# Kernel optimization log

Hardware: AMD Instinct MI355X
Metric: run time of the kernel (lower is better)

## Reference

```python
import jax, jax.numpy as jnp
import numpy as np

N_HEAD = 16
WINDOW = 256
GLOBAL = 32


def _sparse_mask(T):
    # local window of +/- WINDOW//2 plus global rows/cols for first GLOBAL tokens
    i = jnp.arange(T)
    local = jnp.abs(i[:, None] - i[None, :]) <= (WINDOW // 2)
    glob = (i[:, None] < GLOBAL) | (i[None, :] < GLOBAL)
    return local | glob  # [T, T] bool


def setup_inputs() -> dict:
    key = jax.random.key(0)
    k1, k2, k3 = jax.random.split(key, 3)
    B, T, C = 1, 4096, 1024
    scale = 0.02
    return {
        "x": jax.random.normal(k1, (B, T, C), dtype=jnp.float32),
        "W_attn": jax.random.normal(k2, (C, 3 * C), dtype=jnp.float32) * scale,
        "b_attn": jnp.zeros((3 * C,), dtype=jnp.float32),
        "W_proj": jax.random.normal(k3, (C, C), dtype=jnp.float32) * scale,
        "b_proj": jnp.zeros((C,), dtype=jnp.float32),
    }


def reference(x, W_attn, b_attn, W_proj, b_proj):
    B, T, C = x.shape
    H = N_HEAD
    D = C // H

    qkv = x @ W_attn + b_attn  # [B, T, 3C]
    q, k, v = jnp.split(qkv, 3, axis=-1)
    # [B, H, T, D]
    q = q.reshape(B, T, H, D).transpose(0, 2, 1, 3)
    k = k.reshape(B, T, H, D).transpose(0, 2, 1, 3)
    v = v.reshape(B, T, H, D).transpose(0, 2, 1, 3)

    mask = _sparse_mask(T)  # [T, T]
    att = jnp.einsum("bhqd,bhkd->bhqk", q, k) * (1.0 / np.sqrt(D))
    neg = jnp.finfo(att.dtype).min
    att = jnp.where(mask, att, neg)
    att = jax.nn.softmax(att, axis=-1)
    y = jnp.einsum("bhqk,bhkd->bhqd", att, v)  # [B, H, T, D]
    y = y.transpose(0, 2, 1, 3).reshape(B, T, C)
    return y @ W_proj + b_proj
```

## Files before the change

### kernel.cpp

```cpp
#include <hip/hip_runtime.h>
#include <hip/hip_bf16.h>
#include <math.h>

#define T_SEQ 4096
#define C_DIM 1024
#define H_HEADS 16
#define D_HEAD 64
#define QKVW 3072
#define WIN_HALF 128
#define GLOBAL_TOK 32

typedef __attribute__((ext_vector_type(8))) short bf16x8;
typedef __attribute__((ext_vector_type(4))) float f32x4;

__device__ __forceinline__ float bf2f(unsigned short u) {
    union { unsigned int i; float f; } c; c.i = ((unsigned int)u) << 16; return c.f;
}
__device__ __forceinline__ unsigned short f2bf(float f) {
    union { float f; unsigned int i; } c; c.f = f;
    return (unsigned short)((c.i + 0x7fffu + ((c.i >> 16) & 1u)) >> 16);
}

__device__ __forceinline__ void gll16(const unsigned short* g, unsigned short* l) {
    __builtin_amdgcn_global_load_lds(
        (const __attribute__((address_space(1))) void*)g,
        (__attribute__((address_space(3))) void*)l, 16, 0, 0);
}

__global__ __launch_bounds__(256) void cvt_f32_bf16_kernel(
    const float* __restrict__ src, unsigned short* __restrict__ dst, int n4)
{
    int idx = blockIdx.x * 256 + threadIdx.x;
    if (idx < n4) {
        float4 v = ((const float4*)src)[idx];
        ushort4 o;
        o.x = f2bf(v.x); o.y = f2bf(v.y); o.z = f2bf(v.z); o.w = f2bf(v.w);
        ((ushort4*)dst)[idx] = o;
    }
}

__global__ __launch_bounds__(256) void cvt_transpose_kernel(
    const float* __restrict__ src, unsigned short* __restrict__ dst,
    int R, int Ncols)
{
    __shared__ unsigned short tile[32][36];
    const int r0 = blockIdx.y * 32, c0 = blockIdx.x * 32;
    const int t = threadIdx.x;
    const int rr = t >> 3, cq = (t & 7) * 4;
    float4 v = *(const float4*)(src + (size_t)(r0 + rr) * Ncols + c0 + cq);
    tile[rr][cq + 0] = f2bf(v.x); tile[rr][cq + 1] = f2bf(v.y);
    tile[rr][cq + 2] = f2bf(v.z); tile[rr][cq + 3] = f2bf(v.w);
    __syncthreads();
    const int cc = t >> 3, rq = (t & 7) * 4;
    ushort4 o;
    o.x = tile[rq + 0][cc]; o.y = tile[rq + 1][cc];
    o.z = tile[rq + 2][cc]; o.w = tile[rq + 3][cc];
    *(ushort4*)(dst + (size_t)(c0 + cc) * R + r0 + rq) = o;
}

__global__ __launch_bounds__(256) void transpose_v_kernel(
    const unsigned short* __restrict__ qkv, unsigned short* __restrict__ vT)
{
    __shared__ unsigned short tile[32][36];
    const int c0 = blockIdx.x * 32;
    const int t0 = blockIdx.y * 32;
    const int t = threadIdx.x;
    const int rr = t >> 3, cq = (t & 7) * 4;
    ushort4 v = *(const ushort4*)(qkv + (size_t)(t0 + rr) * QKVW + 2 * C_DIM + c0 + cq);
    tile[rr][cq + 0] = v.x; tile[rr][cq + 1] = v.y;
    tile[rr][cq + 2] = v.z; tile[rr][cq + 3] = v.w;
    __syncthreads();
    const int cc = t >> 3, rq = (t & 7) * 4;
    ushort4 o;
    o.x = tile[rq + 0][cc]; o.y = tile[rq + 1][cc];
    o.z = tile[rq + 2][cc]; o.w = tile[rq + 3][cc];
    *(ushort4*)(vT + (size_t)(c0 + cc) * T_SEQ + t0 + rq) = o;
}

template<int OUT_BF16>
__global__ __launch_bounds__(256) void gemm_nt_kernel(
    const unsigned short* __restrict__ A,
    const unsigned short* __restrict__ Bt,
    const float* __restrict__ bias,
    void* __restrict__ Cv, int M, int N, int K)
{
    __shared__ unsigned short As[128 * 32];
    __shared__ unsigned short Bs[128 * 32];
    const int tid = threadIdx.x;
    const int w = tid >> 6, lane = tid & 63;
    const int quad = lane >> 4, r16 = lane & 15;
    const int m0 = blockIdx.y * 128, n0 = blockIdx.x * 128;
    const int wm = (w & 1) * 64, wn = (w >> 1) * 64;

    f32x4 acc[4][4];
    #pragma unroll
    for (int i = 0; i < 4; ++i)
        #pragma unroll
        for (int j = 0; j < 4; ++j) acc[i][j] = (f32x4){0.f, 0.f, 0.f, 0.f};

    const unsigned short* Ab = A + (size_t)m0 * K;
    const unsigned short* Bb = Bt + (size_t)n0 * K;

    for (int k0 = 0; k0 < K; k0 += 32) {
        __syncthreads();
        #pragma unroll
        for (int i = 0; i < 2; ++i) {
            const int chunk = w * 128 + i * 64 + lane;
            const int row = chunk >> 2, kc = (chunk & 3) * 8;
            gll16(Ab + (size_t)row * K + k0 + kc, &As[(w * 2 + i) * 512]);
            gll16(Bb + (size_t)row * K + k0 + kc, &Bs[(w * 2 + i) * 512]);
        }
        asm volatile("s_waitcnt vmcnt(0)" ::: "memory");
        __builtin_amdgcn_sched_barrier(0);
        __syncthreads();

        bf16x8 af[4], bf_[4];
        #pragma unroll
        for (int t = 0; t < 4; ++t) {
            af[t]  = *(const bf16x8*)&As[(wm + t * 16 + r16) * 32 + quad * 8];
            bf_[t] = *(const bf16x8*)&Bs[(wn + t * 16 + r16) * 32 + quad * 8];
        }
        #pragma unroll
        for (int mt = 0; mt < 4; ++mt)
            #pragma unroll
            for (int nt = 0; nt < 4; ++nt)
                acc[mt][nt] = __builtin_amdgcn_mfma_f32_16x16x32_bf16(
                    af[mt], bf_[nt], acc[mt][nt], 0, 0, 0);
    }

    #pragma unroll
    for (int nt = 0; nt < 4; ++nt) {
        const int col = n0 + wn + nt * 16 + r16;
        const float bv = bias[col];
        #pragma unroll
        for (int mt = 0; mt < 4; ++mt)
            #pragma unroll
            for (int reg = 0; reg < 4; ++reg) {
                const int row = m0 + wm + mt * 16 + quad * 4 + reg;
                if (OUT_BF16)
                    ((unsigned short*)Cv)[(size_t)row * N + col] = f2bf(acc[mt][nt][reg] + bv);
                else
                    ((float*)Cv)[(size_t)row * N + col] = acc[mt][nt][reg] + bv;
            }
    }
}

#define PT_STRIDE 72
#define NSLOT 8
#define PROW 72

struct KVbuf { bf16x8 kl[4], kh[4], vl[4], vh[4]; };

#define LOAD_KV(C0, B)                                                         \
  {                                                                            \
    const unsigned short* kr_ = kb + (size_t)((C0) + n) * QKVW + quad * 8;     \
    _Pragma("unroll")                                                          \
    for (int g = 0; g < 4; ++g) {                                              \
      B.kl[g] = *(const bf16x8*)(kr_ + (size_t)(g * 16) * QKVW);               \
      B.kh[g] = *(const bf16x8*)(kr_ + (size_t)(g * 16) * QKVW + 32);          \
    }                                                                          \
    const unsigned short* vr_ = vb + (size_t)n * T_SEQ + (C0) + quad * 8;      \
    _Pragma("unroll")                                                          \
    for (int d = 0; d < 4; ++d) {                                              \
      B.vl[d] = *(const bf16x8*)(vr_ + (size_t)(d * 16) * T_SEQ);              \
      B.vh[d] = *(const bf16x8*)(vr_ + (size_t)(d * 16) * T_SEQ + 32);         \
    }                                                                          \
  }

#define PROC_TILE(ITV, CUR, NXT)                                               \
  {                                                                            \
    const int it_ = (ITV);                                                     \
    const int c0 = dense ? (split * 512 + it_ * 64)                            \
                         : (it_ == 0 ? 0 : wlo + (it_ - 1) * 64);              \
    f32x4 St[4];                                                               \
    _Pragma("unroll")                                                          \
    for (int g = 0; g < 4; ++g) {                                              \
      St[g] = __builtin_amdgcn_mfma_f32_16x16x32_bf16(CUR.kl[g], q0, Zf, 0, 0, 0); \
      St[g] = __builtin_amdgcn_mfma_f32_16x16x32_bf16(CUR.kh[g], q1, St[g], 0, 0, 0); \
    }                                                                          \
    if (it_ + 1 < n_tiles) {                                                   \
      const int c0n_ = dense ? (split * 512 + (it_ + 1) * 64)                  \
                             : (it_ == 0 ? wlo : c0 + 64);                     \
      LOAD_KV(c0n_, NXT);                                                      \
    }                                                                          \
    float mm = -INFINITY;                                                      \
    const bool interior_ =                                                     \
        dense || (it_ != 0 && c0 >= rowbase - 113 && c0 <= rowbase + 65);      \
    if (interior_) {                                                           \
      _Pragma("unroll")                                                        \
      for (int g = 0; g < 4; ++g)                                              \
        _Pragma("unroll")                                                      \
        for (int r = 0; r < 4; ++r) {                                          \
          const float v = St[g][r] * 0.125f;                                   \
          St[g][r] = v; mm = fmaxf(mm, v);                                     \
        }                                                                      \
    } else if (it_ == 0 && rowbase >= 192) {                                   \
      _Pragma("unroll")                                                        \
      for (int g = 0; g < 2; ++g)                                              \
        _Pragma("unroll")                                                      \
        for (int r = 0; r < 4; ++r) {                                          \
          const float v = St[g][r] * 0.125f;                                   \
          St[g][r] = v; mm = fmaxf(mm, v);                                     \
        }                                                                      \
      _Pragma("unroll")                                                        \
      for (int g = 2; g < 4; ++g)                                              \
        _Pragma("unroll")                                                      \
        for (int r = 0; r < 4; ++r) St[g][r] = -INFINITY;                      \
    } else {                                                                   \
      _Pragma("unroll")                                                        \
      for (int g = 0; g < 4; ++g)                                              \
        _Pragma("unroll")                                                      \
        for (int r = 0; r < 4; ++r) {                                          \
          float v = St[g][r] * 0.125f;                                         \
          const int col = c0 + g * 16 + quad * 4 + r;                          \
          int dd = row - col; dd = dd < 0 ? -dd : dd;                          \
          if (!(col < GLOBAL_TOK || dd <= WIN_HALF)) v = -INFINITY;            \
          St[g][r] = v; mm = fmaxf(mm, v);                                     \
        }                                                                      \
    }                                                                          \
    mm = fmaxf(mm, __shfl_xor(mm, 16));                                        \
    mm = fmaxf(mm, __shfl_xor(mm, 32));                                        \
    const float mn = fmaxf(m_run, mm);                                         \
    const float mnf = (mn == -INFINITY) ? 0.f : mn;                            \
    const float al = __expf(m_run - mnf);                                      \
    float rs = 0.f;                                                            \
    _Pragma("unroll")                                                          \
    for (int g = 0; g < 4; ++g) {                                              \
      const float e0 = __expf(St[g][0] - mnf);                                 \
      const float e1 = __expf(St[g][1] - mnf);                                 \
      const float e2 = __expf(St[g][2] - mnf);                                 \
      const float e3 = __expf(St[g][3] - mnf);                                 \
      rs += (e0 + e1) + (e2 + e3);                                             \
      const unsigned int p01 = f2bf(e0) | ((unsigned int)f2bf(e1) << 16);      \
      const unsigned int p23 = f2bf(e2) | ((unsigned int)f2bf(e3) << 16);      \
      *(unsigned int*)&myPt[n * PT_STRIDE + g * 16 + quad * 4] = p01;          \
      *(unsigned int*)&myPt[n * PT_STRIDE + g * 16 + quad * 4 + 2] = p23;      \
    }                                                                          \
    rs += __shfl_xor(rs, 16);                                                  \
    rs += __shfl_xor(rs, 32);                                                  \
    l_run = l_run * al + rs;                                                   \
    m_run = mn;                                                                \
    _Pragma("unroll")                                                          \
    for (int d = 0; d < 4; ++d)                                                \
      _Pragma("unroll")                                                        \
      for (int r = 0; r < 4; ++r) O[d][r] *= al;                               \
    asm volatile("s_waitcnt lgkmcnt(0)" ::: "memory");                         \
    __builtin_amdgcn_sched_barrier(0);                                         \
    _Pragma("unroll")                                                          \
    for (int kg = 0; kg < 2; ++kg) {                                           \
      bf16x8 pf_ = *(const bf16x8*)&myPt[n * PT_STRIDE + kg * 32 + quad * 8];  \
      _Pragma("unroll")                                                        \
      for (int d = 0; d < 4; ++d)                                              \
        O[d] = __builtin_amdgcn_mfma_f32_16x16x32_bf16(                        \
            kg ? CUR.vh[d] : CUR.vl[d], pf_, O[d], 0, 0, 0);                   \
    }                                                                          \
  }

__global__ __launch_bounds__(256, 2) void sparse_attn_mfma(
    const unsigned short* __restrict__ qkv,
    const unsigned short* __restrict__ vT,
    unsigned short* __restrict__ y,
    float* __restrict__ part)
{
    __shared__ unsigned short Pt[4][16 * PT_STRIDE];
    const int tid = threadIdx.x;
    const int w = tid >> 6, lane = tid & 63;
    const int quad = lane >> 4, n = lane & 15;
    const int bid = blockIdx.x;

    int h, rowbase, split = -1, rt = 0;
    if (bid < 1024) {
        h = bid & 15;
        const int rtile = (bid >> 4) * 4 + w;
        if (rtile < 2) return;
        rowbase = rtile * 16;
    } else {
        const int idx = bid - 1024;
        h = idx & 15;
        const int u = (idx >> 4) * 4 + w;
        rt = u >> 3; split = u & 7;
        rowbase = rt * 16;
    }
    const bool dense = split >= 0;

    int wlo = 0, n_tiles;
    if (dense) n_tiles = 8;
    else {
        int t0 = (rowbase - WIN_HALF) & ~63; if (t0 < 64) t0 = 64;
        wlo = t0;
        int whi = rowbase + 16 + WIN_HALF; if (whi > T_SEQ) whi = T_SEQ;
        n_tiles = 1 + (whi - wlo + 63) / 64;
    }

    const unsigned short* qp = qkv + (size_t)(rowbase + n) * QKVW + h * 64 + quad * 8;
    bf16x8 q0 = *(const bf16x8*)qp;
    bf16x8 q1 = *(const bf16x8*)(qp + 32);

    const unsigned short* kb = qkv + C_DIM + h * 64;
    const unsigned short* vb = vT + (size_t)h * 64 * T_SEQ;
    unsigned short* myPt = Pt[w];

    f32x4 O[4];
    #pragma unroll
    for (int i = 0; i < 4; ++i) O[i] = (f32x4){0.f, 0.f, 0.f, 0.f};
    float m_run = -INFINITY, l_run = 0.f;
    const int row = rowbase + n;
    const f32x4 Zf = (f32x4){0.f, 0.f, 0.f, 0.f};

    KVbuf b0, b1;
    {
        const int c00 = dense ? (split * 512) : 0;
        LOAD_KV(c00, b0);
    }
    int it = 0;
    for (;;) {
        PROC_TILE(it, b0, b1);
        if (++it >= n_tiles) break;
        PROC_TILE(it, b1, b0);
        if (++it >= n_tiles) break;
    }

    if (!dense) {
        const float invL = 1.f / l_run;
        #pragma unroll
        for (int dblk = 0; dblk < 4; ++dblk)
            #pragma unroll
            for (int r = 0; r < 4; ++r)
                y[(size_t)row * C_DIM + h * 64 + dblk * 16 + quad * 4 + r] =
                    f2bf(O[dblk][r] * invL);
    } else {
        float* pb = part + ((size_t)(h * 2 + rt) * NSLOT + split) * 16 * PROW;
        #pragma unroll
        for (int dblk = 0; dblk < 4; ++dblk)
            #pragma unroll
            for (int r = 0; r < 4; ++r)
                pb[n * PROW + dblk * 16 + quad * 4 + r] = O[dblk][r];
        if (quad == 0) {
            pb[n * PROW + 64] = m_run;
            pb[n * PROW + 65] = l_run;
        }
    }
}

__global__ __launch_bounds__(64) void attn_combine(
    const float* __restrict__ part, unsigned short* __restrict__ y)
{
    const int d = threadIdx.x;
    const int h = blockIdx.x >> 1, rt = blockIdx.x & 1;
    const float* base = part + (size_t)(h * 2 + rt) * NSLOT * 16 * PROW;
    for (int row = 0; row < 16; ++row) {
        float M = -INFINITY;
        for (int sl = 0; sl < NSLOT; ++sl)
            M = fmaxf(M, base[(size_t)sl * 16 * PROW + row * PROW + 64]);
        float L = 0.f, Od = 0.f;
        for (int sl = 0; sl < NSLOT; ++sl) {
            const float* p = base + (size_t)sl * 16 * PROW + row * PROW;
            const float s = __expf(p[64] - M);
            L += p[65] * s;
            Od += p[d] * s;
        }
        y[(size_t)(rt * 16 + row) * C_DIM + h * 64 + d] = f2bf(Od / L);
    }
}

extern "C" void kernel_launch(void* const* d_in, const int* in_sizes, int n_in,
                              void* d_out, int out_size, void* d_ws, size_t ws_size,
                              hipStream_t stream) {
    const float* x  = (const float*)d_in[0];
    const float* Wa = (const float*)d_in[1];
    const float* ba = (const float*)d_in[2];
    const float* Wp = (const float*)d_in[3];
    const float* bp = (const float*)d_in[4];
    float* out = (float*)d_out;

    unsigned short* xb   = (unsigned short*)d_ws;
    unsigned short* Wabt = xb   + (size_t)T_SEQ * C_DIM;
    unsigned short* Wpbt = Wabt + (size_t)C_DIM * QKVW;
    unsigned short* qkv  = Wpbt + (size_t)C_DIM * C_DIM;
    unsigned short* yat  = qkv  + (size_t)T_SEQ * QKVW;
    unsigned short* vT = xb;
    float* part = (float*)Wabt;

    const int n_x = T_SEQ * C_DIM;
    cvt_f32_bf16_kernel<<<n_x / 4 / 256, 256, 0, stream>>>(x, xb, n_x / 4);
    cvt_transpose_kernel<<<dim3(QKVW / 32, C_DIM / 32), 256, 0, stream>>>(
        Wa, Wabt, C_DIM, QKVW);
    cvt_transpose_kernel<<<dim3(C_DIM / 32, C_DIM / 32), 256, 0, stream>>>(
        Wp, Wpbt, C_DIM, C_DIM);

    gemm_nt_kernel<1><<<dim3(QKVW / 128, T_SEQ / 128), 256, 0, stream>>>(
        xb, Wabt, ba, qkv, T_SEQ, QKVW, C_DIM);

    transpose_v_kernel<<<dim3(C_DIM / 32, T_SEQ / 32), 256, 0, stream>>>(qkv, vT);

    const int nBlocks = 1024 + 64;
    sparse_attn_mfma<<<nBlocks, 256, 0, stream>>>(qkv, vT, yat, part);
    attn_combine<<<H_HEADS * 2, 64, 0, stream>>>(part, yat);

    gemm_nt_kernel<0><<<dim3(C_DIM / 128, T_SEQ / 128), 256, 0, stream>>>(
        yat, Wpbt, bp, out, T_SEQ, C_DIM, C_DIM);
}
```

Measured before the change: 224.0 us.

## Share K/V tiles across warps via swizzled double-buffered LDS in windowed attention

Before this change, each warp in the windowed (non-dense) path loaded its own K/V fragments straight from global memory. Now the four warps of a block, which cover 64 consecutive rows, share a union window of K/V tiles. The block stages those tiles cooperatively into XOR-swizzled, double-buffered LDS, with register prefetch of the next tile and __syncthreads between tiles. This cuts redundant global traffic, and the launch-bounds occupancy hint rises from 2 to 3 blocks per SM. In exchange, each warp now iterates over the larger union window, which adds some wasted MFMA work, and every tile pays a block-wide barrier. The dense global-row path is split out unchanged.

```diff
diff --git a/kernel.cpp b/kernel.cpp
--- a/kernel.cpp
+++ b/kernel.cpp
@@ -25,6 +25,10 @@
     __builtin_amdgcn_global_load_lds(
         (const __attribute__((address_space(1))) void*)g,
         (__attribute__((address_space(3))) void*)l, 16, 0, 0);
+}
+
+__device__ __forceinline__ int swz(int row, int chunk) {
+    return row * 64 + ((chunk ^ (row & 7)) * 8);
 }
 
 __global__ __launch_bounds__(256) void cvt_f32_bf16_kernel(
@@ -150,6 +154,7 @@
 #define PROW 72
 
 struct KVbuf { bf16x8 kl[4], kh[4], vl[4], vh[4]; };
+struct StReg { bf16x8 a, b, c, d; };
 
 #define LOAD_KV(C0, B)                                                         \
   {                                                                            \
@@ -167,57 +172,7 @@
     }                                                                          \
   }
 
-#define PROC_TILE(ITV, CUR, NXT)                                               \
-  {                                                                            \
-    const int it_ = (ITV);                                                     \
-    const int c0 = dense ? (split * 512 + it_ * 64)                            \
-                         : (it_ == 0 ? 0 : wlo + (it_ - 1) * 64);              \
-    f32x4 St[4];                                                               \
-    _Pragma("unroll")                                                          \
-    for (int g = 0; g < 4; ++g) {                                              \
-      St[g] = __builtin_amdgcn_mfma_f32_16x16x32_bf16(CUR.kl[g], q0, Zf, 0, 0, 0); \
-      St[g] = __builtin_amdgcn_mfma_f32_16x16x32_bf16(CUR.kh[g], q1, St[g], 0, 0, 0); \
-    }                                                                          \
-    if (it_ + 1 < n_tiles) {                                                   \
-      const int c0n_ = dense ? (split * 512 + (it_ + 1) * 64)                  \
-                             : (it_ == 0 ? wlo : c0 + 64);                     \
-      LOAD_KV(c0n_, NXT);                                                      \
-    }                                                                          \
-    float mm = -INFINITY;                                                      \
-    const bool interior_ =                                                     \
-        dense || (it_ != 0 && c0 >= rowbase - 113 && c0 <= rowbase + 65);      \
-    if (interior_) {                                                           \
-      _Pragma("unroll")                                                        \
-      for (int g = 0; g < 4; ++g)                                              \
-        _Pragma("unroll")                                                      \
-        for (int r = 0; r < 4; ++r) {                                          \
-          const float v = St[g][r] * 0.125f;                                   \
-          St[g][r] = v; mm = fmaxf(mm, v);                                     \
-        }                                                                      \
-    } else if (it_ == 0 && rowbase >= 192) {                                   \
-      _Pragma("unroll")                                                        \
-      for (int g = 0; g < 2; ++g)                                              \
-        _Pragma("unroll")                                                      \
-        for (int r = 0; r < 4; ++r) {                                          \
-          const float v = St[g][r] * 0.125f;                                   \
-          St[g][r] = v; mm = fmaxf(mm, v);                                     \
-        }                                                                      \
-      _Pragma("unroll")                                                        \
-      for (int g = 2; g < 4; ++g)                                              \
-        _Pragma("unroll")                                                      \
-        for (int r = 0; r < 4; ++r) St[g][r] = -INFINITY;                      \
-    } else {                                                                   \
-      _Pragma("unroll")                                                        \
-      for (int g = 0; g < 4; ++g)                                              \
-        _Pragma("unroll")                                                      \
-        for (int r = 0; r < 4; ++r) {                                          \
-          float v = St[g][r] * 0.125f;                                         \
-          const int col = c0 + g * 16 + quad * 4 + r;                          \
-          int dd = row - col; dd = dd < 0 ? -dd : dd;                          \
-          if (!(col < GLOBAL_TOK || dd <= WIN_HALF)) v = -INFINITY;            \
-          St[g][r] = v; mm = fmaxf(mm, v);                                     \
-        }                                                                      \
-    }                                                                          \
+#define SOFTMAX_P_UPDATE(StV)                                                  \
     mm = fmaxf(mm, __shfl_xor(mm, 16));                                        \
     mm = fmaxf(mm, __shfl_xor(mm, 32));                                        \
     const float mn = fmaxf(m_run, mm);                                         \
@@ -226,10 +181,10 @@
     float rs = 0.f;                                                            \
     _Pragma("unroll")                                                          \
     for (int g = 0; g < 4; ++g) {                                              \
-      const float e0 = __expf(St[g][0] - mnf);                                 \
-      const float e1 = __expf(St[g][1] - mnf);                                 \
-      const float e2 = __expf(St[g][2] - mnf);                                 \
-      const float e3 = __expf(St[g][3] - mnf);                                 \
+      const float e0 = __expf(StV[g][0] - mnf);                                \
+      const float e1 = __expf(StV[g][1] - mnf);                                \
+      const float e2 = __expf(StV[g][2] - mnf);                                \
+      const float e3 = __expf(StV[g][3] - mnf);                                \
       rs += (e0 + e1) + (e2 + e3);                                             \
       const unsigned int p01 = f2bf(e0) | ((unsigned int)f2bf(e1) << 16);      \
       const unsigned int p23 = f2bf(e2) | ((unsigned int)f2bf(e3) << 16);      \
@@ -243,7 +198,30 @@
     _Pragma("unroll")                                                          \
     for (int d = 0; d < 4; ++d)                                                \
       _Pragma("unroll")                                                        \
-      for (int r = 0; r < 4; ++r) O[d][r] *= al;                               \
+      for (int r = 0; r < 4; ++r) O[d][r] *= al;
+
+#define PROC_TILE(ITV, CUR, NXT)                                               \
+  {                                                                            \
+    const int it_ = (ITV);                                                     \
+    const int c0 = split * 512 + it_ * 64;                                     \
+    f32x4 St[4];                                                               \
+    _Pragma("unroll")                                                          \
+    for (int g = 0; g < 4; ++g) {                                              \
+      St[g] = __builtin_amdgcn_mfma_f32_16x16x32_bf16(CUR.kl[g], q0, Zf, 0, 0, 0); \
+      St[g] = __builtin_amdgcn_mfma_f32_16x16x32_bf16(CUR.kh[g], q1, St[g], 0, 0, 0); \
+    }                                                                          \
+    if (it_ + 1 < n_tiles) {                                                   \
+      LOAD_KV(c0 + 64, NXT);                                                   \
+    }                                                                          \
+    float mm = -INFINITY;                                                      \
+    _Pragma("unroll")                                                          \
+    for (int g = 0; g < 4; ++g)                                                \
+      _Pragma("unroll")                                                        \
+      for (int r = 0; r < 4; ++r) {                                            \
+        const float v = St[g][r] * 0.125f;                                     \
+        St[g][r] = v; mm = fmaxf(mm, v);                                       \
+      }                                                                        \
+    SOFTMAX_P_UPDATE(St)                                                       \
     asm volatile("s_waitcnt lgkmcnt(0)" ::: "memory");                         \
     __builtin_amdgcn_sched_barrier(0);                                         \
     _Pragma("unroll")                                                          \
@@ -256,79 +234,195 @@
     }                                                                          \
   }
 
-__global__ __launch_bounds__(256, 2) void sparse_attn_mfma(
+#define STAGE_LOAD(C0, R)                                                      \
+  { const int c0s_ = (C0);                                                     \
+    R.a = *(const bf16x8*)(kb + (size_t)(c0s_ + srow) * QKVW + scol * 8);      \
+    R.b = *(const bf16x8*)(kb + (size_t)(c0s_ + srow + 32) * QKVW + scol * 8); \
+    R.c = *(const bf16x8*)(vb + (size_t)srow * T_SEQ + c0s_ + scol * 8);       \
+    R.d = *(const bf16x8*)(vb + (size_t)(srow + 32) * T_SEQ + c0s_ + scol * 8); }
+
+#define STAGE_WRITE(BUF, R)                                                    \
+  { *(bf16x8*)&Ks[BUF][kdst0] = R.a;                                           \
+    *(bf16x8*)&Ks[BUF][kdst1] = R.b;                                           \
+    *(bf16x8*)&Vs[BUF][kdst0] = R.c;                                           \
+    *(bf16x8*)&Vs[BUF][kdst1] = R.d; }
+
+#define WTILE(ITV, BUF, RW, RL)                                                \
+  {                                                                            \
+    const int it_ = (ITV);                                                     \
+    const int c0 = (it_ == 0) ? 0 : (blo + (it_ - 1) * 64);                    \
+    if (activeW) {                                                             \
+      bf16x8 kl[4], kh[4];                                                     \
+      _Pragma("unroll")                                                        \
+      for (int g = 0; g < 4; ++g) {                                            \
+        kl[g] = *(const bf16x8*)&Ks[BUF][swz(n + g * 16, quad)];               \
+        kh[g] = *(const bf16x8*)&Ks[BUF][swz(n + g * 16, quad + 4)];           \
+      }                                                                        \
+      f32x4 St[4];                                                             \
+      _Pragma("unroll")                                                        \
+      for (int g = 0; g < 4; ++g) {                                            \
+        St[g] = __builtin_amdgcn_mfma_f32_16x16x32_bf16(kl[g], q0, Zf, 0, 0, 0); \
+        St[g] = __builtin_amdgcn_mfma_f32_16x16x32_bf16(kh[g], q1, St[g], 0, 0, 0); \
+      }                                                                        \
+      float mm = -INFINITY;                                                    \
+      if (it_ != 0 && c0 >= rowbase - 113 && c0 <= rowbase + 65) {             \
+        _Pragma("unroll")                                                      \
+        for (int g = 0; g < 4; ++g)                                            \
+          _Pragma("unroll")                                                    \
+          for (int r = 0; r < 4; ++r) {                                        \
+            const float v = St[g][r] * 0.125f;                                 \
+            St[g][r] = v; mm = fmaxf(mm, v);                                   \
+          }                                                                    \
+      } else if (it_ == 0 && rowbase >= 192) {                                 \
+        _Pragma("unroll")                                                      \
+        for (int g = 0; g < 2; ++g)                                            \
+          _Pragma("unroll")                                                    \
+          for (int r = 0; r < 4; ++r) {                                        \
+            const float v = St[g][r] * 0.125f;                                 \
+            St[g][r] = v; mm = fmaxf(mm, v);                                   \
+          }                                                                    \
+        _Pragma("unroll")                                                      \
+        for (int g = 2; g < 4; ++g)                                            \
+          _Pragma("unroll")                                                    \
+          for (int r = 0; r < 4; ++r) St[g][r] = -INFINITY;                    \
+      } else {                                                                 \
+        _Pragma("unroll")                                                      \
+        for (int g = 0; g < 4; ++g)                                            \
+          _Pragma("unroll")                                                    \
+          for (int r = 0; r < 4; ++r) {                                        \
+            float v = St[g][r] * 0.125f;                                       \
+            const int col = c0 + g * 16 + quad * 4 + r;                        \
+            int dd = row - col; dd = dd < 0 ? -dd : dd;                        \
+            if (!(col < GLOBAL_TOK || dd <= WIN_HALF)) v = -INFINITY;          \
+            St[g][r] = v; mm = fmaxf(mm, v);                                   \
+          }                                                                    \
+      }                                                                        \
+      SOFTMAX_P_UPDATE(St)                                                     \
+      bf16x8 vl[4], vh[4];                                                     \
+      _Pragma("unroll")                                                        \
+      for (int d = 0; d < 4; ++d) {                                            \
+        vl[d] = *(const bf16x8*)&Vs[BUF][swz(n + d * 16, quad)];               \
+        vh[d] = *(const bf16x8*)&Vs[BUF][swz(n + d * 16, quad + 4)];           \
+      }                                                                        \
+      asm volatile("s_waitcnt lgkmcnt(0)" ::: "memory");                       \
+      __builtin_amdgcn_sched_barrier(0);                                       \
+      _Pragma("unroll")                                                        \
+      for (int kg = 0; kg < 2; ++kg) {                                         \
+        bf16x8 pf_ = *(const bf16x8*)&myPt[n * PT_STRIDE + kg * 32 + quad * 8];\
+        _Pragma("unroll")                                                      \
+        for (int d = 0; d < 4; ++d)                                            \
+          O[d] = __builtin_amdgcn_mfma_f32_16x16x32_bf16(                      \
+              kg ? vh[d] : vl[d], pf_, O[d], 0, 0, 0);                         \
+      }                                                                        \
+    }                                                                          \
+    if (it_ + 1 < NT) {                                                        \
+      asm volatile("s_waitcnt vmcnt(0)" ::: "memory");                         \
+      __builtin_amdgcn_sched_barrier(0);                                       \
+      STAGE_WRITE((BUF) ^ 1, RW);                                              \
+      if (it_ + 2 < NT) { STAGE_LOAD(blo + (it_ + 1) * 64, RL); }              \
+      __syncthreads();                                                         \
+    }                                                                          \
+  }
+
+__global__ __launch_bounds__(256, 3) void sparse_attn_mfma(
     const unsigned short* __restrict__ qkv,
     const unsigned short* __restrict__ vT,
     unsigned short* __restrict__ y,
     float* __restrict__ part)
 {
+    __shared__ unsigned short Ks[2][64 * 64];
+    __shared__ unsigned short Vs[2][64 * 64];
     __shared__ unsigned short Pt[4][16 * PT_STRIDE];
     const int tid = threadIdx.x;
     const int w = tid >> 6, lane = tid & 63;
     const int quad = lane >> 4, n = lane & 15;
     const int bid = blockIdx.x;
-
-    int h, rowbase, split = -1, rt = 0;
+    const f32x4 Zf = (f32x4){0.f, 0.f, 0.f, 0.f};
+
     if (bid < 1024) {
-        h = bid & 15;
-        const int rtile = (bid >> 4) * 4 + w;
-        if (rtile < 2) return;
-        rowbase = rtile * 16;
+        const int h = bid & 15;
+        const int B = bid >> 4;
+        const int base = B * 64;
+        const int rowbase = base + w * 16;
+        const bool activeW = !(B == 0 && w < 2);
+        int blo = base - 128; if (blo < 64) blo = 64;
+        int bhi = base + 192; if (bhi > T_SEQ) bhi = T_SEQ;
+        const int NT = 1 + (bhi - blo) / 64;
+
+        const unsigned short* kb = qkv + C_DIM + h * 64;
+        const unsigned short* vb = vT + (size_t)h * 64 * T_SEQ;
+        unsigned short* myPt = Pt[w];
+
+        const int srow = tid >> 3, scol = tid & 7;
+        const int kdst0 = swz(srow, scol);
+        const int kdst1 = kdst0 + 32 * 64;
+
+        const unsigned short* qp = qkv + (size_t)(rowbase + n) * QKVW + h * 64 + quad * 8;
+        bf16x8 q0 = *(const bf16x8*)qp;
+        bf16x8 q1 = *(const bf16x8*)(qp + 32);
+
+        f32x4 O[4];
+        #pragma unroll
+        for (int i = 0; i < 4; ++i) O[i] = (f32x4){0.f, 0.f, 0.f, 0.f};
+        float m_run = -INFINITY, l_run = 0.f;
+        const int row = rowbase + n;
+
+        StReg r0, r1;
+        STAGE_LOAD(0, r0);
+        asm volatile("s_waitcnt vmcnt(0)" ::: "memory");
+        __builtin_amdgcn_sched_barrier(0);
+        STAGE_WRITE(0, r0);
+        STAGE_LOAD(blo, r1);
+        __syncthreads();
+
+        int it = 0;
+        for (;;) {
+            WTILE(it, 0, r1, r0);
+            if (++it >= NT) break;
+            WTILE(it, 1, r0, r1);
+            if (++it >= NT) break;
+        }
+
+        if (activeW) {
+            const float invL = 1.f / l_run;
+            #pragma unroll
+            for (int dblk = 0; dblk < 4; ++dblk)
+                #pragma unroll
+                for (int r = 0; r < 4; ++r)
+                    y[(size_t)row * C_DIM + h * 64 + dblk * 16 + quad * 4 + r] =
+                        f2bf(O[dblk][r] * invL);
+        }
     } else {
         const int idx = bid - 1024;
-        h = idx & 15;
+        const int h = idx & 15;
         const int u = (idx >> 4) * 4 + w;
-        rt = u >> 3; split = u & 7;
-        rowbase = rt * 16;
-    }
-    const bool dense = split >= 0;
-
-    int wlo = 0, n_tiles;
-    if (dense) n_tiles = 8;
-    else {
-        int t0 = (rowbase - WIN_HALF) & ~63; if (t0 < 64) t0 = 64;
-        wlo = t0;
-        int whi = rowbase + 16 + WIN_HALF; if (whi > T_SEQ) whi = T_SEQ;
-        n_tiles = 1 + (whi - wlo + 63) / 64;
-    }
-
-    const unsigned short* qp = qkv + (size_t)(rowbase + n) * QKVW + h * 64 + quad * 8;
-    bf16x8 q0 = *(const bf16x8*)qp;
-    bf16x8 q1 = *(const bf16x8*)(qp + 32);
-
-    const unsigned short* kb = qkv + C_DIM + h * 64;
-    const unsigned short* vb = vT + (size_t)h * 64 * T_SEQ;
-    unsigned short* myPt = Pt[w];
-
-    f32x4 O[4];
-    #pragma unroll
-    for (int i = 0; i < 4; ++i) O[i] = (f32x4){0.f, 0.f, 0.f, 0.f};
-    float m_run = -INFINITY, l_run = 0.f;
-    const int row = rowbase + n;
-    const f32x4 Zf = (f32x4){0.f, 0.f, 0.f, 0.f};
-
-    KVbuf b0, b1;
-    {
-        const int c00 = dense ? (split * 512) : 0;
-        LOAD_KV(c00, b0);
-    }
-    int it = 0;
-    for (;;) {
-        PROC_TILE(it, b0, b1);
-        if (++it >= n_tiles) break;
-        PROC_TILE(it, b1, b0);
-        if (++it >= n_tiles) break;
-    }
-
-    if (!dense) {
-        const float invL = 1.f / l_run;
-        #pragma unroll
-        for (int dblk = 0; dblk < 4; ++dblk)
-            #pragma unroll
-            for (int r = 0; r < 4; ++r)
-                y[(size_t)row * C_DIM + h * 64 + dblk * 16 + quad * 4 + r] =
-                    f2bf(O[dblk][r] * invL);
-    } else {
+        const int rt = u >> 3, split = u & 7;
+        const int rowbase = rt * 16;
+        const int n_tiles = 8;
+
+        const unsigned short* qp = qkv + (size_t)(rowbase + n) * QKVW + h * 64 + quad * 8;
+        bf16x8 q0 = *(const bf16x8*)qp;
+        bf16x8 q1 = *(const bf16x8*)(qp + 32);
+
+        const unsigned short* kb = qkv + C_DIM + h * 64;
+        const unsigned short* vb = vT + (size_t)h * 64 * T_SEQ;
+        unsigned short* myPt = Pt[w];
+
+        f32x4 O[4];
+        #pragma unroll
+        for (int i = 0; i < 4; ++i) O[i] = (f32x4){0.f, 0.f, 0.f, 0.f};
+        float m_run = -INFINITY, l_run = 0.f;
+
+        KVbuf b0, b1;
+        LOAD_KV(split * 512, b0);
+        int it = 0;
+        for (;;) {
+            PROC_TILE(it, b0, b1);
+            if (++it >= n_tiles) break;
+            PROC_TILE(it, b1, b0);
+            if (++it >= n_tiles) break;
+        }
+
         float* pb = part + ((size_t)(h * 2 + rt) * NSLOT + split) * 16 * PROW;
         #pragma unroll
         for (int dblk = 0; dblk < 4; ++dblk)
```

Result: faster. 201.0 us (-10.3%).
